# Performance work log

Measured on AMD Instinct MI355X. Metric: run time of the kernel, lower is better.

## Reference

```python
import jax, jax.numpy as jnp
import numpy as np

N = 524288
FEAT = 32
RES = 256
BOUNDS = 1.3

OFFSETS = np.array([[-1.0, 0.0], [-0.5, 0.0], [0.5, 0.0], [1.0, 0.0],
                    [0.0, -1.0], [0.0, -0.5], [0.0, 0.5], [0.0, 1.0],
                    [0.5, 0.5], [0.5, -0.5], [-0.5, 0.5], [-0.5, -0.5]],
                   dtype=np.float32)  # [12, 2]


def setup_inputs() -> dict:
    key = jax.random.key(0)
    k = jax.random.split(key, 7)
    pts = (jax.random.uniform(k[0], (N, 3), jnp.float32) * 2.0 - 1.0) * (BOUNDS * 0.9)
    timestamps = jax.random.uniform(k[1], (N,), jnp.float32)
    scales = jax.random.uniform(k[2], (N, 3), jnp.float32) * 0.05
    plane0 = jax.random.normal(k[3], (FEAT, RES, RES), jnp.float32) * 0.1
    plane1 = jax.random.normal(k[4], (FEAT, RES, RES), jnp.float32) * 0.1
    plane2 = jax.random.normal(k[5], (FEAT, RES, RES), jnp.float32) * 0.1
    aabb = jnp.array([[BOUNDS, BOUNDS, BOUNDS], [-BOUNDS, -BOUNDS, -BOUNDS]], jnp.float32)
    return {"pts": pts, "timestamps": timestamps, "scales": scales,
            "plane0": plane0, "plane1": plane1, "plane2": plane2, "aabb": aabb}


def _bilinear_sample(plane, xy):
    # plane: [C, H, W]; xy: [M, 2] normalized coords in [-1, 1] (x -> W, y -> H)
    C, H, W = plane.shape
    x = jnp.clip((xy[:, 0] + 1.0) * 0.5 * (W - 1), 0.0, W - 1)
    y = jnp.clip((xy[:, 1] + 1.0) * 0.5 * (H - 1), 0.0, H - 1)
    x0 = jnp.floor(x)
    y0 = jnp.floor(y)
    wx = x - x0
    wy = y - y0
    x0i = x0.astype(jnp.int32)
    y0i = y0.astype(jnp.int32)
    x1i = jnp.minimum(x0i + 1, W - 1)
    y1i = jnp.minimum(y0i + 1, H - 1)
    f00 = plane[:, y0i, x0i]  # [C, M]
    f10 = plane[:, y0i, x1i]
    f01 = plane[:, y1i, x0i]
    f11 = plane[:, y1i, x1i]
    out = (f00 * ((1.0 - wx) * (1.0 - wy)) + f10 * (wx * (1.0 - wy))
           + f01 * ((1.0 - wx) * wy) + f11 * (wx * wy))
    return out.T  # [M, C]


def _interpolate_mul(pts_n, scales, planes):
    offsets = jnp.asarray(OFFSETS)  # [12, 2]
    pairs = ((0, 1), (0, 2), (1, 2))
    interp = 1.0
    for i, (q, r) in enumerate(pairs):
        base = pts_n[:, (q, r)]                                   # [N, 2]
        so = scales[:, (q, r)][:, None, :] * offsets[None, :, :]  # [N, 12, 2]
        pts13 = jnp.concatenate([base[:, None, :], base[:, None, :] + so], axis=1)  # [N, 13, 2]
        feat = _bilinear_sample(planes[i], pts13.reshape(-1, 2))  # [N*13, C]
        feat = feat.reshape(-1, 13, feat.shape[-1]).mean(axis=1)  # [N, C]
        interp = interp * feat
    return interp


def reference(pts, timestamps, scales, plane0, plane1, plane2, aabb):
    # normalize_aabb: aabb = [[+b,+b,+b], [-b,-b,-b]]
    pts_n = (pts - aabb[0]) * (2.0 / (aabb[1] - aabb[0])) - 1.0
    pts_n = pts_n.reshape(-1, pts_n.shape[-1])
    del timestamps  # detached / unused in feature interpolation
    return _interpolate_mul(pts_n, scales, (plane0, plane1, plane2))
```

## Files before the change

### kernel.cpp

```cpp
#include <hip/hip_runtime.h>
#include <hip/hip_fp16.h>

#define RES 256
#define FEAT 32
#define PLANE_ELEMS (FEAT * RES * RES)
#define PLANE_BYTES (PLANE_ELEMS * 2)
#define NBINS 32768
#define TQ_BLOCKS (3 * 256 * 4)

typedef unsigned u32x4 __attribute__((ext_vector_type(4)));


__device__ inline unsigned spread3(unsigned v) {
    unsigned r = 0;
    r |= (v & 1u);
    r |= (v & 2u) << 2;
    r |= (v & 4u) << 4;
    r |= (v & 8u) << 6;
    r |= (v & 16u) << 8;
    return r;
}

__global__ __launch_bounds__(256) void pre_tq_hist(const float* __restrict__ p0,
                                                   const float* __restrict__ p1,
                                                   const float* __restrict__ p2,
                                                   __half* __restrict__ outp,
                                                   const float* __restrict__ pts,
                                                   const float* __restrict__ aabb,
                                                   int* __restrict__ hist,
                                                   int* __restrict__ keys, int n) {
    int tid = threadIdx.x;
    if (blockIdx.x < TQ_BLOCKS) {
        __shared__ unsigned lds[64 * 17];
        int bid = blockIdx.x;
        int pl = bid >> 10;
        int rem = bid & 1023;
        int y = rem >> 2;
        int xbase = (rem & 3) * 64;
        const float* in = pl == 0 ? p0 : (pl == 1 ? p1 : p2);

        {
            int x = tid & 63;
            int c2b = (tid >> 6) * 4;
#pragma unroll
            for (int cc = 0; cc < 4; ++cc) {
                int c2 = c2b + cc;
                float f0 = in[(2 * c2) * (RES * RES) + y * RES + xbase + x];
                float f1 = in[(2 * c2 + 1) * (RES * RES) + y * RES + xbase + x];
                unsigned u = (unsigned)__half_as_ushort(__float2half(f0)) |
                             ((unsigned)__half_as_ushort(__float2half(f1)) << 16);
                lds[x * 17 + c2] = u;
            }
        }
        __syncthreads();

        {
            unsigned* o32 = reinterpret_cast<unsigned*>(outp) + (size_t)pl * (PLANE_ELEMS / 2);
            int c2 = tid & 15;
            int xo = (tid >> 4) & 15;
#pragma unroll
            for (int xx = 0; xx < 4; ++xx) {
                int x = xx * 16 + xo;
                o32[(size_t)(y * 256 + xbase + x) * 16 + c2] = lds[x * 17 + c2];
            }
        }
    } else {
        int i = (blockIdx.x - TQ_BLOCKS) * 256 + tid;
        if (i >= n) return;
        float a00 = aabb[0], a01 = aabb[1], a02 = aabb[2];
        float a10 = aabb[3], a11 = aabb[4], a12 = aabb[5];
        float px = (pts[i * 3 + 0] - a00) * (2.0f / (a10 - a00)) - 1.0f;
        float py = (pts[i * 3 + 1] - a01) * (2.0f / (a11 - a01)) - 1.0f;
        float pz = (pts[i * 3 + 2] - a02) * (2.0f / (a12 - a02)) - 1.0f;
        unsigned ux = (unsigned)min(max((int)((px + 1.0f) * 16.0f), 0), 31);
        unsigned uy = (unsigned)min(max((int)((py + 1.0f) * 16.0f), 0), 31);
        unsigned uz = (unsigned)min(max((int)((pz + 1.0f) * 16.0f), 0), 31);
        int key = (int)(spread3(ux) | (spread3(uy) << 1) | (spread3(uz) << 2));
        keys[i] = key;
        atomicAdd(&hist[key], 1);
    }
}

__global__ __launch_bounds__(1024) void scan_hist(int* __restrict__ hist) {
    __shared__ int sums[1024];
    int t = threadIdx.x;
    int base = t * 32;
    int4 L[8];
    const int4* h4 = reinterpret_cast<const int4*>(hist + base);
#pragma unroll
    for (int i = 0; i < 8; ++i) L[i] = h4[i];
    int s = 0;
#pragma unroll
    for (int i = 0; i < 8; ++i) s += L[i].x + L[i].y + L[i].z + L[i].w;
    sums[t] = s;
    __syncthreads();
    for (int off = 1; off < 1024; off <<= 1) {
        int v = 0;
        if (t >= off) v = sums[t - off];
        __syncthreads();
        if (t >= off) sums[t] += v;
        __syncthreads();
    }
    int excl = (t == 0) ? 0 : sums[t - 1];
    int4* o4 = reinterpret_cast<int4*>(hist + base);
#pragma unroll
    for (int i = 0; i < 8; ++i) {
        int4 v;
        v.x = excl; excl += L[i].x;
        v.y = excl; excl += L[i].y;
        v.z = excl; excl += L[i].z;
        v.w = excl; excl += L[i].w;
        o4[i] = v;
    }
}

__global__ __launch_bounds__(256) void scatter_pack(const float* __restrict__ pts,
                                                    const float* __restrict__ scales,
                                                    const float* __restrict__ aabb,
                                                    const int* __restrict__ keys,
                                                    int* __restrict__ hist,
                                                    float* __restrict__ ppk,
                                                    int* __restrict__ idx_s, int n) {
    int i = blockIdx.x * 256 + threadIdx.x;
    if (i >= n) return;
    float a00 = aabb[0], a01 = aabb[1], a02 = aabb[2];
    float a10 = aabb[3], a11 = aabb[4], a12 = aabb[5];
    float px = (pts[i * 3 + 0] - a00) * (2.0f / (a10 - a00)) - 1.0f;
    float py = (pts[i * 3 + 1] - a01) * (2.0f / (a11 - a01)) - 1.0f;
    float pz = (pts[i * 3 + 2] - a02) * (2.0f / (a12 - a02)) - 1.0f;
    int pos = atomicAdd(&hist[keys[i]], 1);
    float4* o = reinterpret_cast<float4*>(ppk) + (size_t)pos * 2;
    o[0] = make_float4((px + 1.0f) * 127.5f, (py + 1.0f) * 127.5f, (pz + 1.0f) * 127.5f, 0.0f);
    o[1] = make_float4(scales[i * 3 + 0] * 63.75f, scales[i * 3 + 1] * 63.75f,
                       scales[i * 3 + 2] * 63.75f, 0.0f);
    idx_s[pos] = i;
}


#define MIX2(f0, f1, d, w)                                                              \
    asm("v_fma_mix_f32 %0, %1, %2, %0 op_sel_hi:[1,0,0]" : "+v"(f0) : "v"(d), "v"(w)); \
    asm("v_fma_mix_f32 %0, %1, %2, %0 op_sel:[1,0,0] op_sel_hi:[1,0,0]" : "+v"(f1) : "v"(d), "v"(w))

__device__ __forceinline__ void mix8(float* fs, u32x4 v, float w) {
    MIX2(fs[0], fs[1], v[0], w);
    MIX2(fs[2], fs[3], v[1], w);
    MIX2(fs[4], fs[5], v[2], w);
    MIX2(fs[6], fs[7], v[3], w);
}

__global__ __launch_bounds__(256) void wpf_main4(const float* __restrict__ ppk,
                                                 const int* __restrict__ idx_s,
                                                 const __half* __restrict__ planes,
                                                 float* __restrict__ out, int n, int swizzle) {
    int b = blockIdx.x;
    if (swizzle) {
        int nb = gridDim.x;
        int chunk = nb >> 3;
        b = (b & 7) * chunk + (b >> 3);
    }
    int t = b * 256 + threadIdx.x;
    int pt = t >> 2;
    int cg = t & 3;
    if (pt >= n) return;

    float4 a  = reinterpret_cast<const float4*>(ppk)[(size_t)pt * 2];
    float4 hh = reinterpret_cast<const float4*>(ppk)[(size_t)pt * 2 + 1];
    int chan = cg * 16;

    const int SI[13] = {2, 0, 1, 3, 4, 2, 2, 2, 2, 3, 3, 1, 1};
    const int SJ[13] = {2, 2, 2, 2, 2, 0, 1, 3, 4, 3, 1, 3, 1};

    float wx[2][5], wy[2][5];
    int   cA[2][5], rA[2][5];
    float fs[8] = {0, 0, 0, 0, 0, 0, 0, 0};
    float interp[8];
    u32x4 X0, X1, X2, X3, Y0, Y1, Y2, Y3, Z0, Z1, Z2, Z3;

#define SETUP(SET, CX, CY, HX, HY, POFF)                 \
    _Pragma("unroll")                                    \
    for (int k = 0; k < 5; ++k) {                        \
        float x_ = fmaf((float)(k - 2), (HX), (CX));     \
        int xi_ = (int)x_;               \
        wx[SET][k] = x_ - (float)xi_;                    \
        cA[SET][k] = xi_ * 64 + chan;                    \
        float y_ = fmaf((float)(k - 2), (HY), (CY));     \
        int yi_ = (int)y_;                               \
        wy[SET][k] = y_ - (float)yi_;                    \
        rA[SET][k] = yi_ * (RES * 64) + (POFF);          \
    }

#define ISSUE(d0, d1, d2, d3, SET, M)                                                     \
    {                                                                                     \
        unsigned vo0_ = (unsigned)(rA[SET][SJ[M]] + cA[SET][SI[M]]);                      \
        unsigned vo1_ = vo0_ + 16384u;                                                    \
        asm volatile("global_load_dwordx4 %0, %1, %2"           : "=v"(d0) : "v"(vo0_), "s"(planes)); \
        asm volatile("global_load_dwordx4 %0, %1, %2 offset:64" : "=v"(d1) : "v"(vo0_), "s"(planes)); \
        asm volatile("global_load_dwordx4 %0, %1, %2"           : "=v"(d2) : "v"(vo1_), "s"(planes)); \
        asm volatile("global_load_dwordx4 %0, %1, %2 offset:64" : "=v"(d3) : "v"(vo1_), "s"(planes)); \
    }
#define WAIT8(b0, b1, b2, b3) \
    asm volatile("s_waitcnt vmcnt(8)" : "+v"(b0), "+v"(b1), "+v"(b2), "+v"(b3))
#define WAIT4(b0, b1, b2, b3) \
    asm volatile("s_waitcnt vmcnt(4)" : "+v"(b0), "+v"(b1), "+v"(b2), "+v"(b3))
#define WAITZ(b0, b1, b2, b3) \
    asm volatile("s_waitcnt vmcnt(0)" : "+v"(b0), "+v"(b1), "+v"(b2), "+v"(b3))
#define CONSUME(SET, M, b0, b1, b2, b3)                  \
    {                                                    \
        float wxi = wx[SET][SI[M]], wyj = wy[SET][SJ[M]];\
        float wxc = 1.0f - wxi, wyc = 1.0f - wyj;        \
        mix8(fs, b0, wxc * wyc);                         \
        mix8(fs, b1, wxi * wyc);                         \
        mix8(fs, b2, wxc * wyj);                         \
        mix8(fs, b3, wxi * wyj);                         \
    }
#define STEP(CS, CSET, ISET, C0, C1, C2, C3, N0, N1, N2, N3) \
    ISSUE(N0, N1, N2, N3, ISET, ((CS) + 2) % 13);            \
    WAIT8(C0, C1, C2, C3);                                   \
    CONSUME(CSET, (CS) % 13, C0, C1, C2, C3);

        SETUP(0, a.x, a.y, hh.x, hh.y, 0)
        ISSUE(X0, X1, X2, X3, 0, 0);
        ISSUE(Y0, Y1, Y2, Y3, 0, 1);
        STEP(0,  0, 0, X0, X1, X2, X3, Z0, Z1, Z2, Z3)
        STEP(1,  0, 0, Y0, Y1, Y2, Y3, X0, X1, X2, X3)
        STEP(2,  0, 0, Z0, Z1, Z2, Z3, Y0, Y1, Y2, Y3)
        STEP(3,  0, 0, X0, X1, X2, X3, Z0, Z1, Z2, Z3)
        STEP(4,  0, 0, Y0, Y1, Y2, Y3, X0, X1, X2, X3)
        STEP(5,  0, 0, Z0, Z1, Z2, Z3, Y0, Y1, Y2, Y3)
        STEP(6,  0, 0, X0, X1, X2, X3, Z0, Z1, Z2, Z3)
        STEP(7,  0, 0, Y0, Y1, Y2, Y3, X0, X1, X2, X3)
        STEP(8,  0, 0, Z0, Z1, Z2, Z3, Y0, Y1, Y2, Y3)
        STEP(9,  0, 0, X0, X1, X2, X3, Z0, Z1, Z2, Z3)
        STEP(10, 0, 0, Y0, Y1, Y2, Y3, X0, X1, X2, X3)
        SETUP(1, a.x, a.z, hh.x, hh.z, PLANE_BYTES)
        STEP(11, 0, 1, Z0, Z1, Z2, Z3, Y0, Y1, Y2, Y3)
        STEP(12, 0, 1, X0, X1, X2, X3, Z0, Z1, Z2, Z3)
#pragma unroll
        for (int c = 0; c < 8; ++c) { interp[c] = fs[c]; fs[c] = 0.0f; }
        STEP(13, 1, 1, Y0, Y1, Y2, Y3, X0, X1, X2, X3)
        STEP(14, 1, 1, Z0, Z1, Z2, Z3, Y0, Y1, Y2, Y3)
        STEP(15, 1, 1, X0, X1, X2, X3, Z0, Z1, Z2, Z3)
        STEP(16, 1, 1, Y0, Y1, Y2, Y3, X0, X1, X2, X3)
        STEP(17, 1, 1, Z0, Z1, Z2, Z3, Y0, Y1, Y2, Y3)
        STEP(18, 1, 1, X0, X1, X2, X3, Z0, Z1, Z2, Z3)
        STEP(19, 1, 1, Y0, Y1, Y2, Y3, X0, X1, X2, X3)
        STEP(20, 1, 1, Z0, Z1, Z2, Z3, Y0, Y1, Y2, Y3)
        STEP(21, 1, 1, X0, X1, X2, X3, Z0, Z1, Z2, Z3)
        STEP(22, 1, 1, Y0, Y1, Y2, Y3, X0, X1, X2, X3)
        STEP(23, 1, 1, Z0, Z1, Z2, Z3, Y0, Y1, Y2, Y3)
        SETUP(0, a.y, a.z, hh.y, hh.z, 2 * PLANE_BYTES)
        STEP(24, 1, 0, X0, X1, X2, X3, Z0, Z1, Z2, Z3)
        STEP(25, 1, 0, Y0, Y1, Y2, Y3, X0, X1, X2, X3)
#pragma unroll
        for (int c = 0; c < 8; ++c) { interp[c] *= fs[c]; fs[c] = 0.0f; }
        STEP(26, 0, 0, Z0, Z1, Z2, Z3, Y0, Y1, Y2, Y3)
        STEP(27, 0, 0, X0, X1, X2, X3, Z0, Z1, Z2, Z3)
        STEP(28, 0, 0, Y0, Y1, Y2, Y3, X0, X1, X2, X3)
        STEP(29, 0, 0, Z0, Z1, Z2, Z3, Y0, Y1, Y2, Y3)
        STEP(30, 0, 0, X0, X1, X2, X3, Z0, Z1, Z2, Z3)
        STEP(31, 0, 0, Y0, Y1, Y2, Y3, X0, X1, X2, X3)
        STEP(32, 0, 0, Z0, Z1, Z2, Z3, Y0, Y1, Y2, Y3)
        STEP(33, 0, 0, X0, X1, X2, X3, Z0, Z1, Z2, Z3)
        STEP(34, 0, 0, Y0, Y1, Y2, Y3, X0, X1, X2, X3)
        STEP(35, 0, 0, Z0, Z1, Z2, Z3, Y0, Y1, Y2, Y3)
        STEP(36, 0, 0, X0, X1, X2, X3, Z0, Z1, Z2, Z3)
        WAIT4(Y0, Y1, Y2, Y3);
        CONSUME(0, 11, Y0, Y1, Y2, Y3);
        WAITZ(Z0, Z1, Z2, Z3);
        CONSUME(0, 12, Z0, Z1, Z2, Z3);

#undef SETUP
#undef ISSUE
#undef WAIT8
#undef WAIT4
#undef WAITZ
#undef CONSUME
#undef STEP

    const float inv = 1.0f / 2197.0f;
    int oi = idx_s[pt];
    float4* o = reinterpret_cast<float4*>(out + (size_t)oi * 32 + cg * 8);
    o[0] = make_float4(interp[0] * fs[0] * inv, interp[1] * fs[1] * inv,
                       interp[2] * fs[2] * inv, interp[3] * fs[3] * inv);
    o[1] = make_float4(interp[4] * fs[4] * inv, interp[5] * fs[5] * inv,
                       interp[6] * fs[6] * inv, interp[7] * fs[7] * inv);
}

__global__ __launch_bounds__(256) void wpf_plain(const float* __restrict__ pts,
                                                 const float* __restrict__ scales,
                                                 const float* __restrict__ p0,
                                                 const float* __restrict__ p1,
                                                 const float* __restrict__ p2,
                                                 const float* __restrict__ aabb,
                                                 float* __restrict__ out, int n) {
    const float offx[13] = {0.f, -1.f, -0.5f, 0.5f, 1.f, 0.f, 0.f, 0.f, 0.f, 0.5f, 0.5f, -0.5f, -0.5f};
    const float offy[13] = {0.f, 0.f, 0.f, 0.f, 0.f, -1.f, -0.5f, 0.5f, 1.f, 0.5f, -0.5f, 0.5f, -0.5f};
    int t = blockIdx.x * 256 + threadIdx.x;
    int pt = t >> 3;
    int cg = t & 7;
    if (pt >= n) return;
    float a00 = aabb[0], a01 = aabb[1], a02 = aabb[2];
    float a10 = aabb[3], a11 = aabb[4], a12 = aabb[5];
    float px = (pts[pt * 3 + 0] - a00) * (2.0f / (a10 - a00)) - 1.0f;
    float py = (pts[pt * 3 + 1] - a01) * (2.0f / (a11 - a01)) - 1.0f;
    float pz = (pts[pt * 3 + 2] - a02) * (2.0f / (a12 - a02)) - 1.0f;
    float scx = scales[pt * 3 + 0], scy = scales[pt * 3 + 1], scz = scales[pt * 3 + 2];
    float4 interp = make_float4(1.f, 1.f, 1.f, 1.f);
    for (int pair = 0; pair < 3; ++pair) {
        const float* plane = pair == 0 ? p0 : (pair == 1 ? p1 : p2);
        float bx = pair == 2 ? py : px;
        float by = pair == 0 ? py : pz;
        float sx = pair == 2 ? scy : scx;
        float sy = pair == 0 ? scy : scz;
        float4 featsum = make_float4(0.f, 0.f, 0.f, 0.f);
        for (int s = 0; s < 13; ++s) {
            float x = fminf(fmaxf((bx + sx * offx[s] + 1.0f) * 127.5f, 0.0f), 255.0f);
            float y = fminf(fmaxf((by + sy * offy[s] + 1.0f) * 127.5f, 0.0f), 255.0f);
            float x0f = floorf(x), y0f = floorf(y);
            float wx = x - x0f, wy = y - y0f;
            int x0 = (int)x0f, y0 = (int)y0f;
            int x1 = min(x0 + 1, RES - 1), y1 = min(y0 + 1, RES - 1);
            float w00 = (1.0f - wx) * (1.0f - wy), w10 = wx * (1.0f - wy);
            float w01 = (1.0f - wx) * wy, w11 = wx * wy;
            int c0 = cg << 2;
            for (int c = 0; c < 4; ++c) {
                const float* pl = plane + (size_t)(c0 + c) * (RES * RES);
                float f = pl[y0 * RES + x0] * w00 + pl[y0 * RES + x1] * w10 +
                          pl[y1 * RES + x0] * w01 + pl[y1 * RES + x1] * w11;
                (&featsum.x)[c] += f;
            }
        }
        const float inv13 = 1.0f / 13.0f;
        interp.x *= featsum.x * inv13;
        interp.y *= featsum.y * inv13;
        interp.z *= featsum.z * inv13;
        interp.w *= featsum.w * inv13;
    }
    reinterpret_cast<float4*>(out)[(size_t)pt * 8 + cg] = interp;
}

extern "C" void kernel_launch(void* const* d_in, const int* in_sizes, int n_in,
                              void* d_out, int out_size, void* d_ws, size_t ws_size,
                              hipStream_t stream) {
    const float* pts    = (const float*)d_in[0];
    const float* scales = (const float*)d_in[2];
    const float* p0     = (const float*)d_in[3];
    const float* p1     = (const float*)d_in[4];
    const float* p2     = (const float*)d_in[5];
    const float* aabb   = (const float*)d_in[6];
    float* out = (float*)d_out;

    int n = in_sizes[0] / 3;
    int pt_blocks = (n + 255) / 256;

    size_t planes_hbytes = (size_t)3 * PLANE_ELEMS * sizeof(__half);
    size_t ppk_bytes = (size_t)n * 8 * sizeof(float);
    size_t idx_bytes = (size_t)n * sizeof(int);
    size_t key_bytes = (size_t)n * sizeof(int);
    size_t hist_bytes = (size_t)NBINS * sizeof(int);
    size_t need = planes_hbytes + ppk_bytes + idx_bytes + key_bytes + hist_bytes;

    if (ws_size >= need) {
        __half* planes_h = (__half*)d_ws;
        float*  ppk   = (float*)((char*)d_ws + planes_hbytes);
        int*    idx_s = (int*)((char*)ppk + ppk_bytes);
        int*    keys  = idx_s + n;
        int*    hist  = keys + n;

        hipMemsetAsync(hist, 0, hist_bytes, stream);
        pre_tq_hist<<<TQ_BLOCKS + pt_blocks, 256, 0, stream>>>(p0, p1, p2, planes_h,
                                                               pts, aabb, hist, keys, n);
        scan_hist<<<1, 1024, 0, stream>>>(hist);
        scatter_pack<<<pt_blocks, 256, 0, stream>>>(pts, scales, aabb, keys, hist,
                                                    ppk, idx_s, n);
        int main_blocks = (n * 4 + 255) / 256;
        int swizzle = (main_blocks % 8 == 0) ? 1 : 0;
        wpf_main4<<<main_blocks, 256, 0, stream>>>(ppk, idx_s, planes_h, out, n, swizzle);
    } else {
        int main_blocks = (n * 8 + 255) / 256;
        wpf_plain<<<main_blocks, 256, 0, stream>>>(pts, scales, p0, p1, p2, aabb, out, n);
    }
}
```

Measured before the change: 318.6 us.

## Fuse preprocessing, histogram scan and scatter into one cooperative kernel

Replaces the three preprocessing launches (plane transpose/fp16 conversion with histogram, single-block scan, scatter/pack) with a single cooperative kernel. It uses grid-wide syncs for the histogram, a distributed per-block scan and the scatter. This removes two launch gaps and the serial single-block scan, and keeps point coordinates in registers instead of rereading pts and keys. It relies on 1024 blocks being co-resident and falls back to the old path if the cooperative launch fails.

```diff
diff --git a/kernel.cpp b/kernel.cpp
--- a/kernel.cpp
+++ b/kernel.cpp
@@ -1,5 +1,8 @@
 #include <hip/hip_runtime.h>
 #include <hip/hip_fp16.h>
+#include <hip/hip_cooperative_groups.h>
+
+namespace cg = cooperative_groups;
 
 #define RES 256
 #define FEAT 32
@@ -7,6 +10,7 @@
 #define PLANE_BYTES (PLANE_ELEMS * 2)
 #define NBINS 32768
 #define TQ_BLOCKS (3 * 256 * 4)
+#define COOP_BLOCKS 1024
 
 typedef unsigned u32x4 __attribute__((ext_vector_type(4)));
 
@@ -20,6 +24,134 @@
     r |= (v & 16u) << 8;
     return r;
 }
+
+__global__ __launch_bounds__(256, 4) void pre_fused(const float* __restrict__ p0,
+                                                    const float* __restrict__ p1,
+                                                    const float* __restrict__ p2,
+                                                    __half* __restrict__ outp,
+                                                    const float* __restrict__ pts,
+                                                    const float* __restrict__ scales,
+                                                    const float* __restrict__ aabb,
+                                                    int* __restrict__ hist,
+                                                    int* __restrict__ blocksum,
+                                                    float* __restrict__ ppk,
+                                                    int* __restrict__ idx_s, int n) {
+    cg::grid_group grid = cg::this_grid();
+    __shared__ unsigned lds[64 * 17];
+    __shared__ int red[256];
+    int tid = threadIdx.x;
+    int b = blockIdx.x;
+
+    for (int u = b; u < 3072; u += COOP_BLOCKS) {
+        int pl = u >> 10;
+        int rem = u & 1023;
+        int y = rem >> 2;
+        int xbase = (rem & 3) * 64;
+        const float* in = pl == 0 ? p0 : (pl == 1 ? p1 : p2);
+        {
+            int x = tid & 63;
+            int c2b = (tid >> 6) * 4;
+#pragma unroll
+            for (int cc = 0; cc < 4; ++cc) {
+                int c2 = c2b + cc;
+                float f0 = in[(2 * c2) * (RES * RES) + y * RES + xbase + x];
+                float f1 = in[(2 * c2 + 1) * (RES * RES) + y * RES + xbase + x];
+                unsigned uv = (unsigned)__half_as_ushort(__float2half(f0)) |
+                              ((unsigned)__half_as_ushort(__float2half(f1)) << 16);
+                lds[x * 17 + c2] = uv;
+            }
+        }
+        __syncthreads();
+        {
+            unsigned* o32 = reinterpret_cast<unsigned*>(outp) + (size_t)pl * (PLANE_ELEMS / 2);
+            int c2 = tid & 15;
+            int xo = (tid >> 4) & 15;
+#pragma unroll
+            for (int xx = 0; xx < 4; ++xx) {
+                int x = xx * 16 + xo;
+                o32[(size_t)(y * 256 + xbase + x) * 16 + c2] = lds[x * 17 + c2];
+            }
+        }
+        __syncthreads();
+    }
+
+    float a00 = aabb[0], a01 = aabb[1], a02 = aabb[2];
+    float a10 = aabb[3], a11 = aabb[4], a12 = aabb[5];
+    float s0 = 2.0f / (a10 - a00), s1 = 2.0f / (a11 - a01), s2 = 2.0f / (a12 - a02);
+    const int STRIDE = COOP_BLOCKS * 256;
+    int gtid = b * 256 + tid;
+    int i0 = gtid, i1 = gtid + STRIDE;
+    bool v0_ = i0 < n, v1_ = i1 < n;
+    float px0 = 0, py0 = 0, pz0 = 0, px1 = 0, py1 = 0, pz1 = 0;
+    int key0 = 0, key1 = 0;
+    if (v0_) {
+        px0 = (pts[i0 * 3 + 0] - a00) * s0 - 1.0f;
+        py0 = (pts[i0 * 3 + 1] - a01) * s1 - 1.0f;
+        pz0 = (pts[i0 * 3 + 2] - a02) * s2 - 1.0f;
+        unsigned ux = (unsigned)min(max((int)((px0 + 1.0f) * 16.0f), 0), 31);
+        unsigned uy = (unsigned)min(max((int)((py0 + 1.0f) * 16.0f), 0), 31);
+        unsigned uz = (unsigned)min(max((int)((pz0 + 1.0f) * 16.0f), 0), 31);
+        key0 = (int)(spread3(ux) | (spread3(uy) << 1) | (spread3(uz) << 2));
+        atomicAdd(&hist[key0], 1);
+    }
+    if (v1_) {
+        px1 = (pts[i1 * 3 + 0] - a00) * s0 - 1.0f;
+        py1 = (pts[i1 * 3 + 1] - a01) * s1 - 1.0f;
+        pz1 = (pts[i1 * 3 + 2] - a02) * s2 - 1.0f;
+        unsigned ux = (unsigned)min(max((int)((px1 + 1.0f) * 16.0f), 0), 31);
+        unsigned uy = (unsigned)min(max((int)((py1 + 1.0f) * 16.0f), 0), 31);
+        unsigned uz = (unsigned)min(max((int)((pz1 + 1.0f) * 16.0f), 0), 31);
+        key1 = (int)(spread3(ux) | (spread3(uy) << 1) | (spread3(uz) << 2));
+        atomicAdd(&hist[key1], 1);
+    }
+    grid.sync();
+
+    int myc = 0, myexcl = 0;
+    if (tid < 32) {
+        myc = hist[b * 32 + tid];
+        int inc = myc;
+#pragma unroll
+        for (int off = 1; off < 32; off <<= 1) {
+            int v = __shfl_up(inc, off, 64);
+            if (tid >= off) inc += v;
+        }
+        myexcl = inc - myc;
+        if (tid == 31) blocksum[b] = inc;
+    }
+    grid.sync();
+
+    int partial = 0;
+    for (int j = tid; j < b; j += 256) partial += blocksum[j];
+    red[tid] = partial;
+    __syncthreads();
+    for (int off = 128; off > 0; off >>= 1) {
+        if (tid < off) red[tid] += red[tid + off];
+        __syncthreads();
+    }
+    int base = red[0];
+    if (tid < 32) hist[b * 32 + tid] = base + myexcl;
+    grid.sync();
+
+    if (v0_) {
+        int pos = atomicAdd(&hist[key0], 1);
+        float4* o = reinterpret_cast<float4*>(ppk) + (size_t)pos * 2;
+        o[0] = make_float4((px0 + 1.0f) * 127.5f, (py0 + 1.0f) * 127.5f,
+                           (pz0 + 1.0f) * 127.5f, 0.0f);
+        o[1] = make_float4(scales[i0 * 3 + 0] * 63.75f, scales[i0 * 3 + 1] * 63.75f,
+                           scales[i0 * 3 + 2] * 63.75f, 0.0f);
+        idx_s[pos] = i0;
+    }
+    if (v1_) {
+        int pos = atomicAdd(&hist[key1], 1);
+        float4* o = reinterpret_cast<float4*>(ppk) + (size_t)pos * 2;
+        o[0] = make_float4((px1 + 1.0f) * 127.5f, (py1 + 1.0f) * 127.5f,
+                           (pz1 + 1.0f) * 127.5f, 0.0f);
+        o[1] = make_float4(scales[i1 * 3 + 0] * 63.75f, scales[i1 * 3 + 1] * 63.75f,
+                           scales[i1 * 3 + 2] * 63.75f, 0.0f);
+        idx_s[pos] = i1;
+    }
+}
+
 
 __global__ __launch_bounds__(256) void pre_tq_hist(const float* __restrict__ p0,
                                                    const float* __restrict__ p1,
@@ -38,7 +170,6 @@
         int y = rem >> 2;
         int xbase = (rem & 3) * 64;
         const float* in = pl == 0 ? p0 : (pl == 1 ? p1 : p2);
-
         {
             int x = tid & 63;
             int c2b = (tid >> 6) * 4;
@@ -53,7 +184,6 @@
             }
         }
         __syncthreads();
-
         {
             unsigned* o32 = reinterpret_cast<unsigned*>(outp) + (size_t)pl * (PLANE_ELEMS / 2);
             int c2 = tid & 15;
@@ -160,12 +290,12 @@
     }
     int t = b * 256 + threadIdx.x;
     int pt = t >> 2;
-    int cg = t & 3;
+    int cg_ = t & 3;
     if (pt >= n) return;
 
     float4 a  = reinterpret_cast<const float4*>(ppk)[(size_t)pt * 2];
     float4 hh = reinterpret_cast<const float4*>(ppk)[(size_t)pt * 2 + 1];
-    int chan = cg * 16;
+    int chan = cg_ * 16;
 
     const int SI[13] = {2, 0, 1, 3, 4, 2, 2, 2, 2, 3, 3, 1, 1};
     const int SJ[13] = {2, 2, 2, 2, 2, 0, 1, 3, 4, 3, 1, 3, 1};
@@ -180,7 +310,7 @@
     _Pragma("unroll")                                    \
     for (int k = 0; k < 5; ++k) {                        \
         float x_ = fmaf((float)(k - 2), (HX), (CX));     \
-        int xi_ = (int)x_;               \
+        int xi_ = (int)x_;                               \
         wx[SET][k] = x_ - (float)xi_;                    \
         cA[SET][k] = xi_ * 64 + chan;                    \
         float y_ = fmaf((float)(k - 2), (HY), (CY));     \
@@ -279,7 +409,7 @@
 
     const float inv = 1.0f / 2197.0f;
     int oi = idx_s[pt];
-    float4* o = reinterpret_cast<float4*>(out + (size_t)oi * 32 + cg * 8);
+    float4* o = reinterpret_cast<float4*>(out + (size_t)oi * 32 + cg_ * 8);
     o[0] = make_float4(interp[0] * fs[0] * inv, interp[1] * fs[1] * inv,
                        interp[2] * fs[2] * inv, interp[3] * fs[3] * inv);
     o[1] = make_float4(interp[4] * fs[4] * inv, interp[5] * fs[5] * inv,
@@ -297,7 +427,7 @@
     const float offy[13] = {0.f, 0.f, 0.f, 0.f, 0.f, -1.f, -0.5f, 0.5f, 1.f, 0.5f, -0.5f, 0.5f, -0.5f};
     int t = blockIdx.x * 256 + threadIdx.x;
     int pt = t >> 3;
-    int cg = t & 7;
+    int cg_ = t & 7;
     if (pt >= n) return;
     float a00 = aabb[0], a01 = aabb[1], a02 = aabb[2];
     float a10 = aabb[3], a11 = aabb[4], a12 = aabb[5];
@@ -322,7 +452,7 @@
             int x1 = min(x0 + 1, RES - 1), y1 = min(y0 + 1, RES - 1);
             float w00 = (1.0f - wx) * (1.0f - wy), w10 = wx * (1.0f - wy);
             float w01 = (1.0f - wx) * wy, w11 = wx * wy;
-            int c0 = cg << 2;
+            int c0 = cg_ << 2;
             for (int c = 0; c < 4; ++c) {
                 const float* pl = plane + (size_t)(c0 + c) * (RES * RES);
                 float f = pl[y0 * RES + x0] * w00 + pl[y0 * RES + x1] * w10 +
@@ -336,7 +466,7 @@
         interp.z *= featsum.z * inv13;
         interp.w *= featsum.w * inv13;
     }
-    reinterpret_cast<float4*>(out)[(size_t)pt * 8 + cg] = interp;
+    reinterpret_cast<float4*>(out)[(size_t)pt * 8 + cg_] = interp;
 }
 
 extern "C" void kernel_launch(void* const* d_in, const int* in_sizes, int n_in,
@@ -358,7 +488,8 @@
     size_t idx_bytes = (size_t)n * sizeof(int);
     size_t key_bytes = (size_t)n * sizeof(int);
     size_t hist_bytes = (size_t)NBINS * sizeof(int);
-    size_t need = planes_hbytes + ppk_bytes + idx_bytes + key_bytes + hist_bytes;
+    size_t bsum_bytes = (size_t)COOP_BLOCKS * sizeof(int);
+    size_t need = planes_hbytes + ppk_bytes + idx_bytes + key_bytes + hist_bytes + bsum_bytes;
 
     if (ws_size >= need) {
         __half* planes_h = (__half*)d_ws;
@@ -366,13 +497,26 @@
         int*    idx_s = (int*)((char*)ppk + ppk_bytes);
         int*    keys  = idx_s + n;
         int*    hist  = keys + n;
+        int*    bsum  = hist + NBINS;
 
         hipMemsetAsync(hist, 0, hist_bytes, stream);
-        pre_tq_hist<<<TQ_BLOCKS + pt_blocks, 256, 0, stream>>>(p0, p1, p2, planes_h,
-                                                               pts, aabb, hist, keys, n);
-        scan_hist<<<1, 1024, 0, stream>>>(hist);
-        scatter_pack<<<pt_blocks, 256, 0, stream>>>(pts, scales, aabb, keys, hist,
-                                                    ppk, idx_s, n);
+
+        hipError_t cerr = hipErrorUnknown;
+        if (n <= 2 * COOP_BLOCKS * 256) {
+            void* args[] = {(void*)&p0, (void*)&p1, (void*)&p2, (void*)&planes_h,
+                            (void*)&pts, (void*)&scales, (void*)&aabb,
+                            (void*)&hist, (void*)&bsum, (void*)&ppk, (void*)&idx_s,
+                            (void*)&n};
+            cerr = hipLaunchCooperativeKernel((void*)pre_fused, dim3(COOP_BLOCKS),
+                                              dim3(256), args, 0, stream);
+        }
+        if (cerr != hipSuccess) {
+            pre_tq_hist<<<TQ_BLOCKS + pt_blocks, 256, 0, stream>>>(p0, p1, p2, planes_h,
+                                                                   pts, aabb, hist, keys, n);
+            scan_hist<<<1, 1024, 0, stream>>>(hist);
+            scatter_pack<<<pt_blocks, 256, 0, stream>>>(pts, scales, aabb, keys, hist,
+                                                        ppk, idx_s, n);
+        }
         int main_blocks = (n * 4 + 255) / 256;
         int swizzle = (main_blocks % 8 == 0) ? 1 : 0;
         wpf_main4<<<main_blocks, 256, 0, stream>>>(ppk, idx_s, planes_h, out, n, swizzle);
```

After: 607.3 us. +90.6%, slower.

## Remove Morton-order point sorting and read points directly in main kernel

Applied to the files above, without the earlier changes.

Drops the histogram, scan and scatter kernels that bucketed points by a 3D Morton key, along with the XCD block swizzle. The main kernel now normalizes points and scales inline from the original arrays and writes output in natural order. This removes three launches, a memset, and the atomics and scatter traffic. In exchange it gives up the spatial locality of plane gathers that sorting provided, which may raise cache misses on random points.

```diff
diff --git a/kernel.cpp b/kernel.cpp
--- a/kernel.cpp
+++ b/kernel.cpp
@@ -5,135 +5,47 @@
 #define FEAT 32
 #define PLANE_ELEMS (FEAT * RES * RES)
 #define PLANE_BYTES (PLANE_ELEMS * 2)
-#define NBINS 32768
-#define TQ_BLOCKS (3 * 256 * 4)
 
 typedef unsigned u32x4 __attribute__((ext_vector_type(4)));
 
 
-__device__ inline unsigned spread3(unsigned v) {
-    unsigned r = 0;
-    r |= (v & 1u);
-    r |= (v & 2u) << 2;
-    r |= (v & 4u) << 4;
-    r |= (v & 8u) << 6;
-    r |= (v & 16u) << 8;
-    return r;
-}
-
-__global__ __launch_bounds__(256) void pre_tq_hist(const float* __restrict__ p0,
-                                                   const float* __restrict__ p1,
-                                                   const float* __restrict__ p2,
-                                                   __half* __restrict__ outp,
-                                                   const float* __restrict__ pts,
-                                                   const float* __restrict__ aabb,
-                                                   int* __restrict__ hist,
-                                                   int* __restrict__ keys, int n) {
+__global__ __launch_bounds__(256) void transpose_quant(const float* __restrict__ p0,
+                                                       const float* __restrict__ p1,
+                                                       const float* __restrict__ p2,
+                                                       __half* __restrict__ outp) {
+    __shared__ unsigned lds[64 * 17];
+    int bid = blockIdx.x;
+    int pl = bid >> 10;
+    int rem = bid & 1023;
+    int y = rem >> 2;
+    int xbase = (rem & 3) * 64;
+    const float* in = pl == 0 ? p0 : (pl == 1 ? p1 : p2);
     int tid = threadIdx.x;
-    if (blockIdx.x < TQ_BLOCKS) {
-        __shared__ unsigned lds[64 * 17];
-        int bid = blockIdx.x;
-        int pl = bid >> 10;
-        int rem = bid & 1023;
-        int y = rem >> 2;
-        int xbase = (rem & 3) * 64;
-        const float* in = pl == 0 ? p0 : (pl == 1 ? p1 : p2);
-
-        {
-            int x = tid & 63;
-            int c2b = (tid >> 6) * 4;
-#pragma unroll
-            for (int cc = 0; cc < 4; ++cc) {
-                int c2 = c2b + cc;
-                float f0 = in[(2 * c2) * (RES * RES) + y * RES + xbase + x];
-                float f1 = in[(2 * c2 + 1) * (RES * RES) + y * RES + xbase + x];
-                unsigned u = (unsigned)__half_as_ushort(__float2half(f0)) |
-                             ((unsigned)__half_as_ushort(__float2half(f1)) << 16);
-                lds[x * 17 + c2] = u;
-            }
+
+    {
+        int x = tid & 63;
+        int c2b = (tid >> 6) * 4;
+#pragma unroll
+        for (int cc = 0; cc < 4; ++cc) {
+            int c2 = c2b + cc;
+            float f0 = in[(2 * c2) * (RES * RES) + y * RES + xbase + x];
+            float f1 = in[(2 * c2 + 1) * (RES * RES) + y * RES + xbase + x];
+            unsigned u = (unsigned)__half_as_ushort(__float2half(f0)) |
+                         ((unsigned)__half_as_ushort(__float2half(f1)) << 16);
+            lds[x * 17 + c2] = u;
         }
-        __syncthreads();
-
-        {
-            unsigned* o32 = reinterpret_cast<unsigned*>(outp) + (size_t)pl * (PLANE_ELEMS / 2);
-            int c2 = tid & 15;
-            int xo = (tid >> 4) & 15;
-#pragma unroll
-            for (int xx = 0; xx < 4; ++xx) {
-                int x = xx * 16 + xo;
-                o32[(size_t)(y * 256 + xbase + x) * 16 + c2] = lds[x * 17 + c2];
-            }
+    }
+    __syncthreads();
+    {
+        unsigned* o32 = reinterpret_cast<unsigned*>(outp) + (size_t)pl * (PLANE_ELEMS / 2);
+        int c2 = tid & 15;
+        int xo = (tid >> 4) & 15;
+#pragma unroll
+        for (int xx = 0; xx < 4; ++xx) {
+            int x = xx * 16 + xo;
+            o32[(size_t)(y * 256 + xbase + x) * 16 + c2] = lds[x * 17 + c2];
         }
-    } else {
-        int i = (blockIdx.x - TQ_BLOCKS) * 256 + tid;
-        if (i >= n) return;
-        float a00 = aabb[0], a01 = aabb[1], a02 = aabb[2];
-        float a10 = aabb[3], a11 = aabb[4], a12 = aabb[5];
-        float px = (pts[i * 3 + 0] - a00) * (2.0f / (a10 - a00)) - 1.0f;
-        float py = (pts[i * 3 + 1] - a01) * (2.0f / (a11 - a01)) - 1.0f;
-        float pz = (pts[i * 3 + 2] - a02) * (2.0f / (a12 - a02)) - 1.0f;
-        unsigned ux = (unsigned)min(max((int)((px + 1.0f) * 16.0f), 0), 31);
-        unsigned uy = (unsigned)min(max((int)((py + 1.0f) * 16.0f), 0), 31);
-        unsigned uz = (unsigned)min(max((int)((pz + 1.0f) * 16.0f), 0), 31);
-        int key = (int)(spread3(ux) | (spread3(uy) << 1) | (spread3(uz) << 2));
-        keys[i] = key;
-        atomicAdd(&hist[key], 1);
-    }
-}
-
-__global__ __launch_bounds__(1024) void scan_hist(int* __restrict__ hist) {
-    __shared__ int sums[1024];
-    int t = threadIdx.x;
-    int base = t * 32;
-    int4 L[8];
-    const int4* h4 = reinterpret_cast<const int4*>(hist + base);
-#pragma unroll
-    for (int i = 0; i < 8; ++i) L[i] = h4[i];
-    int s = 0;
-#pragma unroll
-    for (int i = 0; i < 8; ++i) s += L[i].x + L[i].y + L[i].z + L[i].w;
-    sums[t] = s;
-    __syncthreads();
-    for (int off = 1; off < 1024; off <<= 1) {
-        int v = 0;
-        if (t >= off) v = sums[t - off];
-        __syncthreads();
-        if (t >= off) sums[t] += v;
-        __syncthreads();
-    }
-    int excl = (t == 0) ? 0 : sums[t - 1];
-    int4* o4 = reinterpret_cast<int4*>(hist + base);
-#pragma unroll
-    for (int i = 0; i < 8; ++i) {
-        int4 v;
-        v.x = excl; excl += L[i].x;
-        v.y = excl; excl += L[i].y;
-        v.z = excl; excl += L[i].z;
-        v.w = excl; excl += L[i].w;
-        o4[i] = v;
-    }
-}
-
-__global__ __launch_bounds__(256) void scatter_pack(const float* __restrict__ pts,
-                                                    const float* __restrict__ scales,
-                                                    const float* __restrict__ aabb,
-                                                    const int* __restrict__ keys,
-                                                    int* __restrict__ hist,
-                                                    float* __restrict__ ppk,
-                                                    int* __restrict__ idx_s, int n) {
-    int i = blockIdx.x * 256 + threadIdx.x;
-    if (i >= n) return;
-    float a00 = aabb[0], a01 = aabb[1], a02 = aabb[2];
-    float a10 = aabb[3], a11 = aabb[4], a12 = aabb[5];
-    float px = (pts[i * 3 + 0] - a00) * (2.0f / (a10 - a00)) - 1.0f;
-    float py = (pts[i * 3 + 1] - a01) * (2.0f / (a11 - a01)) - 1.0f;
-    float pz = (pts[i * 3 + 2] - a02) * (2.0f / (a12 - a02)) - 1.0f;
-    int pos = atomicAdd(&hist[keys[i]], 1);
-    float4* o = reinterpret_cast<float4*>(ppk) + (size_t)pos * 2;
-    o[0] = make_float4((px + 1.0f) * 127.5f, (py + 1.0f) * 127.5f, (pz + 1.0f) * 127.5f, 0.0f);
-    o[1] = make_float4(scales[i * 3 + 0] * 63.75f, scales[i * 3 + 1] * 63.75f,
-                       scales[i * 3 + 2] * 63.75f, 0.0f);
-    idx_s[pos] = i;
+    }
 }
 
 
@@ -148,24 +60,28 @@
     MIX2(fs[6], fs[7], v[3], w);
 }
 
-__global__ __launch_bounds__(256) void wpf_main4(const float* __restrict__ ppk,
-                                                 const int* __restrict__ idx_s,
+__global__ __launch_bounds__(256) void wpf_main4(const float* __restrict__ pts,
+                                                 const float* __restrict__ scales,
+                                                 const float* __restrict__ aabb,
                                                  const __half* __restrict__ planes,
-                                                 float* __restrict__ out, int n, int swizzle) {
-    int b = blockIdx.x;
-    if (swizzle) {
-        int nb = gridDim.x;
-        int chunk = nb >> 3;
-        b = (b & 7) * chunk + (b >> 3);
-    }
-    int t = b * 256 + threadIdx.x;
+                                                 float* __restrict__ out, int n) {
+    int t = blockIdx.x * 256 + threadIdx.x;
     int pt = t >> 2;
-    int cg = t & 3;
+    int cg_ = t & 3;
     if (pt >= n) return;
 
-    float4 a  = reinterpret_cast<const float4*>(ppk)[(size_t)pt * 2];
-    float4 hh = reinterpret_cast<const float4*>(ppk)[(size_t)pt * 2 + 1];
-    int chan = cg * 16;
+    float a00 = aabb[0], a01 = aabb[1], a02 = aabb[2];
+    float a10 = aabb[3], a11 = aabb[4], a12 = aabb[5];
+    float pxn = (pts[pt * 3 + 0] - a00) * (2.0f / (a10 - a00)) - 1.0f;
+    float pyn = (pts[pt * 3 + 1] - a01) * (2.0f / (a11 - a01)) - 1.0f;
+    float pzn = (pts[pt * 3 + 2] - a02) * (2.0f / (a12 - a02)) - 1.0f;
+    float cpx = (pxn + 1.0f) * 127.5f;
+    float cpy = (pyn + 1.0f) * 127.5f;
+    float cpz = (pzn + 1.0f) * 127.5f;
+    float hpx = scales[pt * 3 + 0] * 63.75f;
+    float hpy = scales[pt * 3 + 1] * 63.75f;
+    float hpz = scales[pt * 3 + 2] * 63.75f;
+    int chan = cg_ * 16;
 
     const int SI[13] = {2, 0, 1, 3, 4, 2, 2, 2, 2, 3, 3, 1, 1};
     const int SJ[13] = {2, 2, 2, 2, 2, 0, 1, 3, 4, 3, 1, 3, 1};
@@ -218,7 +134,7 @@
     WAIT8(C0, C1, C2, C3);                                   \
     CONSUME(CSET, (CS) % 13, C0, C1, C2, C3);
 
-        SETUP(0, a.x, a.y, hh.x, hh.y, 0)
+        SETUP(0, cpx, cpy, hpx, hpy, 0)
         ISSUE(X0, X1, X2, X3, 0, 0);
         ISSUE(Y0, Y1, Y2, Y3, 0, 1);
         STEP(0,  0, 0, X0, X1, X2, X3, Z0, Z1, Z2, Z3)
@@ -232,7 +148,7 @@
         STEP(8,  0, 0, Z0, Z1, Z2, Z3, Y0, Y1, Y2, Y3)
         STEP(9,  0, 0, X0, X1, X2, X3, Z0, Z1, Z2, Z3)
         STEP(10, 0, 0, Y0, Y1, Y2, Y3, X0, X1, X2, X3)
-        SETUP(1, a.x, a.z, hh.x, hh.z, PLANE_BYTES)
+        SETUP(1, cpx, cpz, hpx, hpz, PLANE_BYTES)
         STEP(11, 0, 1, Z0, Z1, Z2, Z3, Y0, Y1, Y2, Y3)
         STEP(12, 0, 1, X0, X1, X2, X3, Z0, Z1, Z2, Z3)
 #pragma unroll
@@ -248,7 +164,7 @@
         STEP(21, 1, 1, X0, X1, X2, X3, Z0, Z1, Z2, Z3)
         STEP(22, 1, 1, Y0, Y1, Y2, Y3, X0, X1, X2, X3)
         STEP(23, 1, 1, Z0, Z1, Z2, Z3, Y0, Y1, Y2, Y3)
-        SETUP(0, a.y, a.z, hh.y, hh.z, 2 * PLANE_BYTES)
+        SETUP(0, cpy, cpz, hpy, hpz, 2 * PLANE_BYTES)
         STEP(24, 1, 0, X0, X1, X2, X3, Z0, Z1, Z2, Z3)
         STEP(25, 1, 0, Y0, Y1, Y2, Y3, X0, X1, X2, X3)
 #pragma unroll
@@ -278,8 +194,7 @@
 #undef STEP
 
     const float inv = 1.0f / 2197.0f;
-    int oi = idx_s[pt];
-    float4* o = reinterpret_cast<float4*>(out + (size_t)oi * 32 + cg * 8);
+    float4* o = reinterpret_cast<float4*>(out + (size_t)pt * 32 + cg_ * 8);
     o[0] = make_float4(interp[0] * fs[0] * inv, interp[1] * fs[1] * inv,
                        interp[2] * fs[2] * inv, interp[3] * fs[3] * inv);
     o[1] = make_float4(interp[4] * fs[4] * inv, interp[5] * fs[5] * inv,
@@ -297,7 +212,7 @@
     const float offy[13] = {0.f, 0.f, 0.f, 0.f, 0.f, -1.f, -0.5f, 0.5f, 1.f, 0.5f, -0.5f, 0.5f, -0.5f};
     int t = blockIdx.x * 256 + threadIdx.x;
     int pt = t >> 3;
-    int cg = t & 7;
+    int cg_ = t & 7;
     if (pt >= n) return;
     float a00 = aabb[0], a01 = aabb[1], a02 = aabb[2];
     float a10 = aabb[3], a11 = aabb[4], a12 = aabb[5];
@@ -322,7 +237,7 @@
             int x1 = min(x0 + 1, RES - 1), y1 = min(y0 + 1, RES - 1);
             float w00 = (1.0f - wx) * (1.0f - wy), w10 = wx * (1.0f - wy);
             float w01 = (1.0f - wx) * wy, w11 = wx * wy;
-            int c0 = cg << 2;
+            int c0 = cg_ << 2;
             for (int c = 0; c < 4; ++c) {
                 const float* pl = plane + (size_t)(c0 + c) * (RES * RES);
                 float f = pl[y0 * RES + x0] * w00 + pl[y0 * RES + x1] * w10 +
@@ -336,7 +251,7 @@
         interp.z *= featsum.z * inv13;
         interp.w *= featsum.w * inv13;
     }
-    reinterpret_cast<float4*>(out)[(size_t)pt * 8 + cg] = interp;
+    reinterpret_cast<float4*>(out)[(size_t)pt * 8 + cg_] = interp;
 }
 
 extern "C" void kernel_launch(void* const* d_in, const int* in_sizes, int n_in,
@@ -351,31 +266,14 @@
     float* out = (float*)d_out;
 
     int n = in_sizes[0] / 3;
-    int pt_blocks = (n + 255) / 256;
 
     size_t planes_hbytes = (size_t)3 * PLANE_ELEMS * sizeof(__half);
-    size_t ppk_bytes = (size_t)n * 8 * sizeof(float);
-    size_t idx_bytes = (size_t)n * sizeof(int);
-    size_t key_bytes = (size_t)n * sizeof(int);
-    size_t hist_bytes = (size_t)NBINS * sizeof(int);
-    size_t need = planes_hbytes + ppk_bytes + idx_bytes + key_bytes + hist_bytes;
-
-    if (ws_size >= need) {
+
+    if (ws_size >= planes_hbytes) {
         __half* planes_h = (__half*)d_ws;
-        float*  ppk   = (float*)((char*)d_ws + planes_hbytes);
-        int*    idx_s = (int*)((char*)ppk + ppk_bytes);
-        int*    keys  = idx_s + n;
-        int*    hist  = keys + n;
-
-        hipMemsetAsync(hist, 0, hist_bytes, stream);
-        pre_tq_hist<<<TQ_BLOCKS + pt_blocks, 256, 0, stream>>>(p0, p1, p2, planes_h,
-                                                               pts, aabb, hist, keys, n);
-        scan_hist<<<1, 1024, 0, stream>>>(hist);
-        scatter_pack<<<pt_blocks, 256, 0, stream>>>(pts, scales, aabb, keys, hist,
-                                                    ppk, idx_s, n);
+        transpose_quant<<<3 * 256 * 4, 256, 0, stream>>>(p0, p1, p2, planes_h);
         int main_blocks = (n * 4 + 255) / 256;
-        int swizzle = (main_blocks % 8 == 0) ? 1 : 0;
-        wpf_main4<<<main_blocks, 256, 0, stream>>>(ppk, idx_s, planes_h, out, n, swizzle);
+        wpf_main4<<<main_blocks, 256, 0, stream>>>(pts, scales, aabb, planes_h, out, n);
     } else {
         int main_blocks = (n * 8 + 255) / 256;
         wpf_plain<<<main_blocks, 256, 0, stream>>>(pts, scales, p0, p1, p2, aabb, out, n);
```

After: 449.8 us. +41.2%, slower.

## Fold histogram scan into pre-pass via last-block-done pattern; recompute keys

Applied to the files above, without the earlier changes.

Merges the separate single-block scan kernel into the fused transpose/histogram kernel: each block bumps a completion counter, and the last block to finish performs the 32768-bin exclusive scan using 256 threads. The keys array is dropped, and scatter_pack recomputes the Morton key from the point coordinates instead of reading it back. This removes one kernel launch and the key write/read traffic. In exchange the scan runs on 256 threads with serial 128-element loops over atomic loads, which may be slower than the previous 1024-thread vectorized scan.

```diff
diff --git a/kernel.cpp b/kernel.cpp
--- a/kernel.cpp
+++ b/kernel.cpp
@@ -21,17 +21,20 @@
     return r;
 }
 
-__global__ __launch_bounds__(256) void pre_tq_hist(const float* __restrict__ p0,
-                                                   const float* __restrict__ p1,
-                                                   const float* __restrict__ p2,
-                                                   __half* __restrict__ outp,
-                                                   const float* __restrict__ pts,
-                                                   const float* __restrict__ aabb,
-                                                   int* __restrict__ hist,
-                                                   int* __restrict__ keys, int n) {
+__global__ __launch_bounds__(256) void pre_tq_hist_scan(const float* __restrict__ p0,
+                                                        const float* __restrict__ p1,
+                                                        const float* __restrict__ p2,
+                                                        __half* __restrict__ outp,
+                                                        const float* __restrict__ pts,
+                                                        const float* __restrict__ aabb,
+                                                        int* __restrict__ hist,
+                                                        int* __restrict__ done, int n) {
+    __shared__ unsigned lds[64 * 17];
+    __shared__ int sums[256];
+    __shared__ int lastflag;
     int tid = threadIdx.x;
+
     if (blockIdx.x < TQ_BLOCKS) {
-        __shared__ unsigned lds[64 * 17];
         int bid = blockIdx.x;
         int pl = bid >> 10;
         int rem = bid & 1023;
@@ -53,7 +56,6 @@
             }
         }
         __syncthreads();
-
         {
             unsigned* o32 = reinterpret_cast<unsigned*>(outp) + (size_t)pl * (PLANE_ELEMS / 2);
             int c2 = tid & 15;
@@ -66,58 +68,50 @@
         }
     } else {
         int i = (blockIdx.x - TQ_BLOCKS) * 256 + tid;
-        if (i >= n) return;
-        float a00 = aabb[0], a01 = aabb[1], a02 = aabb[2];
-        float a10 = aabb[3], a11 = aabb[4], a12 = aabb[5];
-        float px = (pts[i * 3 + 0] - a00) * (2.0f / (a10 - a00)) - 1.0f;
-        float py = (pts[i * 3 + 1] - a01) * (2.0f / (a11 - a01)) - 1.0f;
-        float pz = (pts[i * 3 + 2] - a02) * (2.0f / (a12 - a02)) - 1.0f;
-        unsigned ux = (unsigned)min(max((int)((px + 1.0f) * 16.0f), 0), 31);
-        unsigned uy = (unsigned)min(max((int)((py + 1.0f) * 16.0f), 0), 31);
-        unsigned uz = (unsigned)min(max((int)((pz + 1.0f) * 16.0f), 0), 31);
-        int key = (int)(spread3(ux) | (spread3(uy) << 1) | (spread3(uz) << 2));
-        keys[i] = key;
-        atomicAdd(&hist[key], 1);
-    }
-}
-
-__global__ __launch_bounds__(1024) void scan_hist(int* __restrict__ hist) {
-    __shared__ int sums[1024];
-    int t = threadIdx.x;
-    int base = t * 32;
-    int4 L[8];
-    const int4* h4 = reinterpret_cast<const int4*>(hist + base);
-#pragma unroll
-    for (int i = 0; i < 8; ++i) L[i] = h4[i];
+        if (i < n) {
+            float a00 = aabb[0], a01 = aabb[1], a02 = aabb[2];
+            float a10 = aabb[3], a11 = aabb[4], a12 = aabb[5];
+            float px = (pts[i * 3 + 0] - a00) * (2.0f / (a10 - a00)) - 1.0f;
+            float py = (pts[i * 3 + 1] - a01) * (2.0f / (a11 - a01)) - 1.0f;
+            float pz = (pts[i * 3 + 2] - a02) * (2.0f / (a12 - a02)) - 1.0f;
+            unsigned ux = (unsigned)min(max((int)((px + 1.0f) * 16.0f), 0), 31);
+            unsigned uy = (unsigned)min(max((int)((py + 1.0f) * 16.0f), 0), 31);
+            unsigned uz = (unsigned)min(max((int)((pz + 1.0f) * 16.0f), 0), 31);
+            int key = (int)(spread3(ux) | (spread3(uy) << 1) | (spread3(uz) << 2));
+            atomicAdd(&hist[key], 1);
+        }
+    }
+
+    __syncthreads();
+    __threadfence();
+    if (tid == 0) lastflag = (atomicAdd(done, 1) == (int)gridDim.x - 1) ? 1 : 0;
+    __syncthreads();
+    if (!lastflag) return;
+    __threadfence();
+
+    int base = tid * 128;
     int s = 0;
-#pragma unroll
-    for (int i = 0; i < 8; ++i) s += L[i].x + L[i].y + L[i].z + L[i].w;
-    sums[t] = s;
+    for (int j = 0; j < 128; ++j)
+        s += __hip_atomic_load(&hist[base + j], __ATOMIC_RELAXED, __HIP_MEMORY_SCOPE_AGENT);
+    sums[tid] = s;
     __syncthreads();
-    for (int off = 1; off < 1024; off <<= 1) {
-        int v = 0;
-        if (t >= off) v = sums[t - off];
+    for (int off = 1; off < 256; off <<= 1) {
+        int v = (tid >= off) ? sums[tid - off] : 0;
         __syncthreads();
-        if (t >= off) sums[t] += v;
+        if (tid >= off) sums[tid] += v;
         __syncthreads();
     }
-    int excl = (t == 0) ? 0 : sums[t - 1];
-    int4* o4 = reinterpret_cast<int4*>(hist + base);
-#pragma unroll
-    for (int i = 0; i < 8; ++i) {
-        int4 v;
-        v.x = excl; excl += L[i].x;
-        v.y = excl; excl += L[i].y;
-        v.z = excl; excl += L[i].z;
-        v.w = excl; excl += L[i].w;
-        o4[i] = v;
+    int excl = (tid == 0) ? 0 : sums[tid - 1];
+    for (int j = 0; j < 128; ++j) {
+        int c = __hip_atomic_load(&hist[base + j], __ATOMIC_RELAXED, __HIP_MEMORY_SCOPE_AGENT);
+        __hip_atomic_store(&hist[base + j], excl, __ATOMIC_RELAXED, __HIP_MEMORY_SCOPE_AGENT);
+        excl += c;
     }
 }
 
 __global__ __launch_bounds__(256) void scatter_pack(const float* __restrict__ pts,
                                                     const float* __restrict__ scales,
                                                     const float* __restrict__ aabb,
-                                                    const int* __restrict__ keys,
                                                     int* __restrict__ hist,
                                                     float* __restrict__ ppk,
                                                     int* __restrict__ idx_s, int n) {
@@ -128,7 +122,11 @@
     float px = (pts[i * 3 + 0] - a00) * (2.0f / (a10 - a00)) - 1.0f;
     float py = (pts[i * 3 + 1] - a01) * (2.0f / (a11 - a01)) - 1.0f;
     float pz = (pts[i * 3 + 2] - a02) * (2.0f / (a12 - a02)) - 1.0f;
-    int pos = atomicAdd(&hist[keys[i]], 1);
+    unsigned ux = (unsigned)min(max((int)((px + 1.0f) * 16.0f), 0), 31);
+    unsigned uy = (unsigned)min(max((int)((py + 1.0f) * 16.0f), 0), 31);
+    unsigned uz = (unsigned)min(max((int)((pz + 1.0f) * 16.0f), 0), 31);
+    int key = (int)(spread3(ux) | (spread3(uy) << 1) | (spread3(uz) << 2));
+    int pos = atomicAdd(&hist[key], 1);
     float4* o = reinterpret_cast<float4*>(ppk) + (size_t)pos * 2;
     o[0] = make_float4((px + 1.0f) * 127.5f, (py + 1.0f) * 127.5f, (pz + 1.0f) * 127.5f, 0.0f);
     o[1] = make_float4(scales[i * 3 + 0] * 63.75f, scales[i * 3 + 1] * 63.75f,
@@ -160,12 +158,12 @@
     }
     int t = b * 256 + threadIdx.x;
     int pt = t >> 2;
-    int cg = t & 3;
+    int cg_ = t & 3;
     if (pt >= n) return;
 
     float4 a  = reinterpret_cast<const float4*>(ppk)[(size_t)pt * 2];
     float4 hh = reinterpret_cast<const float4*>(ppk)[(size_t)pt * 2 + 1];
-    int chan = cg * 16;
+    int chan = cg_ * 16;
 
     const int SI[13] = {2, 0, 1, 3, 4, 2, 2, 2, 2, 3, 3, 1, 1};
     const int SJ[13] = {2, 2, 2, 2, 2, 0, 1, 3, 4, 3, 1, 3, 1};
@@ -279,7 +277,7 @@
 
     const float inv = 1.0f / 2197.0f;
     int oi = idx_s[pt];
-    float4* o = reinterpret_cast<float4*>(out + (size_t)oi * 32 + cg * 8);
+    float4* o = reinterpret_cast<float4*>(out + (size_t)oi * 32 + cg_ * 8);
     o[0] = make_float4(interp[0] * fs[0] * inv, interp[1] * fs[1] * inv,
                        interp[2] * fs[2] * inv, interp[3] * fs[3] * inv);
     o[1] = make_float4(interp[4] * fs[4] * inv, interp[5] * fs[5] * inv,
@@ -297,7 +295,7 @@
     const float offy[13] = {0.f, 0.f, 0.f, 0.f, 0.f, -1.f, -0.5f, 0.5f, 1.f, 0.5f, -0.5f, 0.5f, -0.5f};
     int t = blockIdx.x * 256 + threadIdx.x;
     int pt = t >> 3;
-    int cg = t & 7;
+    int cg_ = t & 7;
     if (pt >= n) return;
     float a00 = aabb[0], a01 = aabb[1], a02 = aabb[2];
     float a10 = aabb[3], a11 = aabb[4], a12 = aabb[5];
@@ -322,7 +320,7 @@
             int x1 = min(x0 + 1, RES - 1), y1 = min(y0 + 1, RES - 1);
             float w00 = (1.0f - wx) * (1.0f - wy), w10 = wx * (1.0f - wy);
             float w01 = (1.0f - wx) * wy, w11 = wx * wy;
-            int c0 = cg << 2;
+            int c0 = cg_ << 2;
             for (int c = 0; c < 4; ++c) {
                 const float* pl = plane + (size_t)(c0 + c) * (RES * RES);
                 float f = pl[y0 * RES + x0] * w00 + pl[y0 * RES + x1] * w10 +
@@ -336,7 +334,7 @@
         interp.z *= featsum.z * inv13;
         interp.w *= featsum.w * inv13;
     }
-    reinterpret_cast<float4*>(out)[(size_t)pt * 8 + cg] = interp;
+    reinterpret_cast<float4*>(out)[(size_t)pt * 8 + cg_] = interp;
 }
 
 extern "C" void kernel_launch(void* const* d_in, const int* in_sizes, int n_in,
@@ -356,22 +354,20 @@
     size_t planes_hbytes = (size_t)3 * PLANE_ELEMS * sizeof(__half);
     size_t ppk_bytes = (size_t)n * 8 * sizeof(float);
     size_t idx_bytes = (size_t)n * sizeof(int);
-    size_t key_bytes = (size_t)n * sizeof(int);
-    size_t hist_bytes = (size_t)NBINS * sizeof(int);
-    size_t need = planes_hbytes + ppk_bytes + idx_bytes + key_bytes + hist_bytes;
+    size_t hist_bytes = (size_t)(NBINS + 1) * sizeof(int);
+    size_t need = planes_hbytes + ppk_bytes + idx_bytes + hist_bytes;
 
     if (ws_size >= need) {
         __half* planes_h = (__half*)d_ws;
         float*  ppk   = (float*)((char*)d_ws + planes_hbytes);
         int*    idx_s = (int*)((char*)ppk + ppk_bytes);
-        int*    keys  = idx_s + n;
-        int*    hist  = keys + n;
+        int*    hist  = idx_s + n;
+        int*    done  = hist + NBINS;
 
         hipMemsetAsync(hist, 0, hist_bytes, stream);
-        pre_tq_hist<<<TQ_BLOCKS + pt_blocks, 256, 0, stream>>>(p0, p1, p2, planes_h,
-                                                               pts, aabb, hist, keys, n);
-        scan_hist<<<1, 1024, 0, stream>>>(hist);
-        scatter_pack<<<pt_blocks, 256, 0, stream>>>(pts, scales, aabb, keys, hist,
+        pre_tq_hist_scan<<<TQ_BLOCKS + pt_blocks, 256, 0, stream>>>(p0, p1, p2, planes_h,
+                                                                    pts, aabb, hist, done, n);
+        scatter_pack<<<pt_blocks, 256, 0, stream>>>(pts, scales, aabb, hist,
                                                     ppk, idx_s, n);
         int main_blocks = (n * 4 + 255) / 256;
         int swizzle = (main_blocks % 8 == 0) ? 1 : 0;
```

After: 905.9 us. +184.4%, slower.
